# Optimization experiments

Hardware: AMD Instinct MI355X
Metric: run time of the kernel (lower is better)

## Reference

```python
import jax, jax.numpy as jnp
import numpy as np

BOUND = 2.3  # default non-learnable bound


def setup_inputs() -> dict:
    key = jax.random.key(0)
    k1, k2, k3, k4 = jax.random.split(key, 4)
    B, C, H, W = 64, 256, 56, 56
    n_points = 7  # n_regions=6
    x = jax.random.normal(k1, (B, C, H, W), dtype=jnp.float32)
    # learned per-channel breakpoint values (relu-like init would be monotone;
    # random values are fine for a correctness baseline)
    points = jax.random.normal(k2, (C, n_points), dtype=jnp.float32)
    left_diffs = jax.random.normal(k3, (C,), dtype=jnp.float32)
    right_diffs = jax.random.normal(k4, (C,), dtype=jnp.float32)
    return {"x": x, "points": points, "left_diffs": left_diffs, "right_diffs": right_diffs}


def reference(x, points, left_diffs, right_diffs):
    # channelwise PWLU, scalar (non-learnable) bounds
    n_points = points.shape[-1]
    n_regions = n_points - 1
    left_b, right_b = -BOUND, BOUND
    region_len = (right_b - left_b) / n_regions          # scalar
    sim_left = left_b - region_len                        # extra region left of bound

    x_normal = (x - sim_left) / region_len                # [B,C,H,W]
    regions = jnp.clip(x_normal, 0.0, (n_regions + 1) * 1.001).astype(jnp.int32)
    dists = x_normal - regions.astype(x.dtype)

    # per-region slopes table: [C, n_points+1]
    diffs = jnp.concatenate(
        [left_diffs[:, None], points[..., 1:] - points[..., :-1], right_diffs[:, None]],
        axis=-1,
    )
    # points table extended with the effective point left of the left bound: [C, n_points+1]
    false_points = jnp.concatenate([(points[..., 0] - left_diffs)[:, None], points], axis=-1)

    C = points.shape[0]
    ch = jnp.arange(C)[None, :, None, None]               # broadcast channel index
    left_points = false_points[ch, regions]               # gather [B,C,H,W]
    slopes = diffs[ch, regions]
    return left_points + dists * slopes
```

## Files before the change

kernel.cpp:

```cpp
#include <hip/hip_runtime.h>


constexpr int NP  = 7;
constexpr int NT  = 8;
constexpr int CH  = 256;
constexpr int HW  = 56 * 56;
constexpr int HW4 = HW / 4;

typedef float f4 __attribute__((ext_vector_type(4)));

__device__ __forceinline__ float pwlu1(float xv, const float2* tbl,
                                       float sim_left, float inv_len, float hi) {
    const float xn = (xv - sim_left) * inv_len;
    const int   r  = (int)fminf(fmaxf(xn, 0.0f), hi);
    const float2 t = tbl[r];
    return fmaf(xn - (float)r, t.y, t.x);
}

__device__ __forceinline__ f4 pwlu4(f4 v, const float2* tbl,
                                    float sim_left, float inv_len, float hi) {
    f4 o;
    o.x = pwlu1(v.x, tbl, sim_left, inv_len, hi);
    o.y = pwlu1(v.y, tbl, sim_left, inv_len, hi);
    o.z = pwlu1(v.z, tbl, sim_left, inv_len, hi);
    o.w = pwlu1(v.w, tbl, sim_left, inv_len, hi);
    return o;
}

__global__ __launch_bounds__(256) void pwlu_kernel(
    const f4* __restrict__ x,
    const float* __restrict__ points,
    const float* __restrict__ left_diffs,
    const float* __restrict__ right_diffs,
    f4* __restrict__ out)
{
    __shared__ float2 tbl[NT];

    const int plane = blockIdx.x;
    const int c     = plane & (CH - 1);
    const int tid   = threadIdx.x;
    const size_t base = (size_t)plane * HW4;

    const f4* __restrict__ xp = x + base + tid;
    f4 v0 = __builtin_nontemporal_load(xp);
    f4 v1 = __builtin_nontemporal_load(xp + 256);
    f4 v2 = __builtin_nontemporal_load(xp + 512);
    const bool tail = tid < (HW4 - 3 * 256);
    f4 v3;
    if (tail) v3 = __builtin_nontemporal_load(xp + 768);

    if (tid < NT) {
        const int r = tid;
        const float* p = points + c * NP;
        float fp, df;
        if (r == 0) {
            const float ld = left_diffs[c];
            fp = p[0] - ld; df = ld;
        } else if (r == NP) {
            fp = p[NP - 1]; df = right_diffs[c];
        } else {
            const float a = p[r - 1], b = p[r];
            fp = a; df = b - a;
        }
        tbl[r] = make_float2(fp, df);
    }
    __syncthreads();

    const float sim_left = -3.0666666666666664f;
    const float inv_len  = 1.3043478260869565f;
    const float hi       = 7.007f;

    f4* __restrict__ op = out + base + tid;
    __builtin_nontemporal_store(pwlu4(v0, tbl, sim_left, inv_len, hi), op);
    __builtin_nontemporal_store(pwlu4(v1, tbl, sim_left, inv_len, hi), op + 256);
    __builtin_nontemporal_store(pwlu4(v2, tbl, sim_left, inv_len, hi), op + 512);
    if (tail)
        __builtin_nontemporal_store(pwlu4(v3, tbl, sim_left, inv_len, hi), op + 768);
}

extern "C" void kernel_launch(void* const* d_in, const int* in_sizes, int n_in,
                              void* d_out, int out_size, void* d_ws, size_t ws_size,
                              hipStream_t stream) {
    const f4*    x  = (const f4*)d_in[0];
    const float* pt = (const float*)d_in[1];
    const float* ld = (const float*)d_in[2];
    const float* rd = (const float*)d_in[3];
    f4*          o  = (f4*)d_out;

    const int planes = in_sizes[0] / HW;
    pwlu_kernel<<<planes, 256, 0, stream>>>(x, pt, ld, rd, o);
}
```

Before: 325.2 us.

## Process 16 planes per block with double-buffered software-pipelined loads

Each block now handles 16 channel planes instead of one, building a full per-channel lookup table in shared memory and streaming the data through a double-buffered register pipeline of seven float4 loads per stage. The aim is to cut the number of blocks, amortise table setup and the barrier, and keep more loads in flight to hide memory latency. In exchange it needs more registers per thread and a larger shared table, and it computes the plane index per element with an integer division.

```diff
diff --git a/kernel.cpp b/kernel.cpp
--- a/kernel.cpp
+++ b/kernel.cpp
@@ -1,81 +1,98 @@
 #include <hip/hip_runtime.h>
 
 
-constexpr int NP  = 7;
-constexpr int NT  = 8;
-constexpr int CH  = 256;
-constexpr int HW  = 56 * 56;
-constexpr int HW4 = HW / 4;
+constexpr int NP   = 7;
+constexpr int NT   = 8;
+constexpr int CH   = 256;
+constexpr int HW   = 56 * 56;
+constexpr int HW4  = HW / 4;
+constexpr int PPB  = 16;
+constexpr int F4PB = PPB * HW4;
+constexpr int UN   = 7;
 
 typedef float f4 __attribute__((ext_vector_type(4)));
 
-__device__ __forceinline__ float pwlu1(float xv, const float2* tbl,
-                                       float sim_left, float inv_len, float hi) {
+__device__ __forceinline__ float pwlu1(float xv, const float2* __restrict__ tc) {
+    constexpr float sim_left = -3.0666666666666664f;
+    constexpr float inv_len  = 1.3043478260869565f;
+    constexpr float hi       = 7.007f;
     const float xn = (xv - sim_left) * inv_len;
     const int   r  = (int)fminf(fmaxf(xn, 0.0f), hi);
-    const float2 t = tbl[r];
+    const float2 t = tc[r];
     return fmaf(xn - (float)r, t.y, t.x);
 }
 
-__device__ __forceinline__ f4 pwlu4(f4 v, const float2* tbl,
-                                    float sim_left, float inv_len, float hi) {
+__device__ __forceinline__ f4 pwlu4(f4 v, const float2* __restrict__ tc) {
     f4 o;
-    o.x = pwlu1(v.x, tbl, sim_left, inv_len, hi);
-    o.y = pwlu1(v.y, tbl, sim_left, inv_len, hi);
-    o.z = pwlu1(v.z, tbl, sim_left, inv_len, hi);
-    o.w = pwlu1(v.w, tbl, sim_left, inv_len, hi);
+    o.x = pwlu1(v.x, tc);
+    o.y = pwlu1(v.y, tc);
+    o.z = pwlu1(v.z, tc);
+    o.w = pwlu1(v.w, tc);
     return o;
 }
 
-__global__ __launch_bounds__(256) void pwlu_kernel(
+template<int IT>
+__device__ __forceinline__ void load7(f4* v, const f4* __restrict__ xp) {
+#pragma unroll
+    for (int j = 0; j < UN; ++j)
+        v[j] = __builtin_nontemporal_load(xp + (IT * UN + j) * 256);
+}
+
+template<int IT>
+__device__ __forceinline__ void proc7(const f4* v, f4* __restrict__ op,
+                                      const float2* __restrict__ tbl,
+                                      int cbase, int tid) {
+#pragma unroll
+    for (int j = 0; j < UN; ++j) {
+        const int idx = IT * UN + j;
+        const int pl  = (int)((unsigned)(idx * 256 + tid) / 784u);
+        const float2* tc = tbl + ((cbase + pl) << 3);
+        __builtin_nontemporal_store(pwlu4(v[j], tc), op + idx * 256);
+    }
+}
+
+__global__ __launch_bounds__(256, 4) void pwlu_kernel(
     const f4* __restrict__ x,
     const float* __restrict__ points,
     const float* __restrict__ left_diffs,
     const float* __restrict__ right_diffs,
     f4* __restrict__ out)
 {
-    __shared__ float2 tbl[NT];
+    __shared__ float2 tbl[CH * NT];
 
-    const int plane = blockIdx.x;
-    const int c     = plane & (CH - 1);
-    const int tid   = threadIdx.x;
-    const size_t base = (size_t)plane * HW4;
+    const int tid = threadIdx.x;
+    const size_t base = (size_t)blockIdx.x * F4PB;
+    const f4* __restrict__ xp = x + base + tid;
+    f4*       __restrict__ op = out + base + tid;
 
-    const f4* __restrict__ xp = x + base + tid;
-    f4 v0 = __builtin_nontemporal_load(xp);
-    f4 v1 = __builtin_nontemporal_load(xp + 256);
-    f4 v2 = __builtin_nontemporal_load(xp + 512);
-    const bool tail = tid < (HW4 - 3 * 256);
-    f4 v3;
-    if (tail) v3 = __builtin_nontemporal_load(xp + 768);
+    f4 va[UN], vb[UN];
+    load7<0>(va, xp);
 
-    if (tid < NT) {
-        const int r = tid;
-        const float* p = points + c * NP;
-        float fp, df;
-        if (r == 0) {
-            const float ld = left_diffs[c];
-            fp = p[0] - ld; df = ld;
-        } else if (r == NP) {
-            fp = p[NP - 1]; df = right_diffs[c];
-        } else {
-            const float a = p[r - 1], b = p[r];
-            fp = a; df = b - a;
+    {
+        const int r  = tid & 7;
+        const int c0 = tid >> 3;
+#pragma unroll
+        for (int k = 0; k < NT; ++k) {
+            const int c = k * 32 + c0;
+            const float* p = points + c * NP;
+            float fp, df;
+            if (r == 0)       { const float ld = left_diffs[c]; fp = p[0] - ld;  df = ld; }
+            else if (r == NP) { fp = p[NP - 1];                  df = right_diffs[c]; }
+            else              { const float a = p[r - 1], b = p[r]; fp = a; df = b - a; }
+            tbl[c * NT + r] = make_float2(fp, df);
         }
-        tbl[r] = make_float2(fp, df);
     }
     __syncthreads();
 
-    const float sim_left = -3.0666666666666664f;
-    const float inv_len  = 1.3043478260869565f;
-    const float hi       = 7.007f;
+    const int cbase = (blockIdx.x & (CH / PPB - 1)) * PPB;
 
-    f4* __restrict__ op = out + base + tid;
-    __builtin_nontemporal_store(pwlu4(v0, tbl, sim_left, inv_len, hi), op);
-    __builtin_nontemporal_store(pwlu4(v1, tbl, sim_left, inv_len, hi), op + 256);
-    __builtin_nontemporal_store(pwlu4(v2, tbl, sim_left, inv_len, hi), op + 512);
-    if (tail)
-        __builtin_nontemporal_store(pwlu4(v3, tbl, sim_left, inv_len, hi), op + 768);
+    load7<1>(vb, xp); proc7<0>(va, op, tbl, cbase, tid);
+    load7<2>(va, xp); proc7<1>(vb, op, tbl, cbase, tid);
+    load7<3>(vb, xp); proc7<2>(va, op, tbl, cbase, tid);
+    load7<4>(va, xp); proc7<3>(vb, op, tbl, cbase, tid);
+    load7<5>(vb, xp); proc7<4>(va, op, tbl, cbase, tid);
+    load7<6>(va, xp); proc7<5>(vb, op, tbl, cbase, tid);
+    proc7<6>(va, op, tbl, cbase, tid);
 }
 
 extern "C" void kernel_launch(void* const* d_in, const int* in_sizes, int n_in,
@@ -88,5 +105,5 @@
     f4*          o  = (f4*)d_out;
 
     const int planes = in_sizes[0] / HW;
-    pwlu_kernel<<<planes, 256, 0, stream>>>(x, pt, ld, rd, o);
+    pwlu_kernel<<<planes / PPB, 256, 0, stream>>>(x, pt, ld, rd, o);
 }
```

After: 343.2 us. 1.06x slower.
